# Kernel optimization log

Hardware: AMD Instinct MI355X
Metric: run time of the kernel (lower is better)

Reference implementation:

```python
import jax, jax.numpy as jnp
import numpy as np

N, IN, C, H, OUT = 100000, 64, 128, 2, 8
D = C // H  # per-head dim = 64
E = 600000
NEG_SLOPE = 0.2


def _edge_softmax(alpha, dst, n):
    # softmax over edges grouped by destination node; alpha: [E,H]
    amax = jax.lax.stop_gradient(jax.ops.segment_max(alpha, dst, num_segments=n))
    amax = jnp.where(jnp.isfinite(amax), amax, 0.0)  # empty segments -> -inf
    e = jnp.exp(alpha - amax[dst])
    s = jax.ops.segment_sum(e, dst, num_segments=n)
    return e / (s[dst] + 1e-16)


def _han_conv(x, edge_list, proj_w, proj_b, att_src, att_dst, q, kw, kb):
    # x: [N, F_in]; edge_list: list of [2,E] int arrays (one per edge type)
    n = x.shape[0]
    h = (x @ proj_w + proj_b).reshape(n, H, D)  # node-type projection
    outs = []
    for i, ei in enumerate(edge_list):  # loop over fixed set of edge types
        src, dst = ei[0], ei[1]
        a_src = (h * att_src[i]).sum(-1)  # [N,H]
        a_dst = (h * att_dst[i]).sum(-1)  # [N,H]
        alpha = jax.nn.leaky_relu(a_src[src] + a_dst[dst], NEG_SLOPE)  # [E,H]
        alpha = _edge_softmax(alpha, dst, n)  # dropout p=0.6 is identity in eval
        msg = h[src] * alpha[..., None]  # [E,H,D]
        out = jax.ops.segment_sum(msg, dst, num_segments=n).reshape(n, C)
        outs.append(jax.nn.relu(out))  # per-edge-type ReLU inside HANConv
    stacked = jnp.stack(outs)  # [M, N, C], M = num edge types
    # semantic-level attention across metapaths
    score = (q * jnp.tanh(stacked @ kw + kb).mean(1)).sum(-1)  # [M]
    attn = jax.nn.softmax(score)
    return (attn[:, None, None] * stacked).sum(0)  # [N, C]


def setup_inputs() -> dict:
    key = jax.random.key(0)
    ks = jax.random.split(key, 16)
    s = 0.1
    d = {}
    d["x"] = jax.random.normal(ks[0], (N, IN), jnp.float32)
    d["ei_spatial"] = jax.random.randint(ks[1], (2, E), 0, N)
    d["ei_similar"] = jax.random.randint(ks[2], (2, E), 0, N)
    # HANConv layer 1 (IN -> C)
    d["p1_proj_w"] = jax.random.normal(ks[3], (IN, C), jnp.float32) * s
    d["p1_proj_b"] = jnp.zeros((C,), jnp.float32)
    d["p1_att_src"] = jax.random.normal(ks[4], (2, H, D), jnp.float32) * s
    d["p1_att_dst"] = jax.random.normal(ks[5], (2, H, D), jnp.float32) * s
    d["p1_q"] = jax.random.normal(ks[6], (C,), jnp.float32) * s
    d["p1_kw"] = jax.random.normal(ks[7], (C, C), jnp.float32) * s
    d["p1_kb"] = jnp.zeros((C,), jnp.float32)
    # HANConv layer 2 (C -> C)
    d["p2_proj_w"] = jax.random.normal(ks[8], (C, C), jnp.float32) * s
    d["p2_proj_b"] = jnp.zeros((C,), jnp.float32)
    d["p2_att_src"] = jax.random.normal(ks[9], (2, H, D), jnp.float32) * s
    d["p2_att_dst"] = jax.random.normal(ks[10], (2, H, D), jnp.float32) * s
    d["p2_q"] = jax.random.normal(ks[11], (C,), jnp.float32) * s
    d["p2_kw"] = jax.random.normal(ks[12], (C, C), jnp.float32) * s
    d["p2_kb"] = jnp.zeros((C,), jnp.float32)
    # final classifier
    d["lin_w"] = jax.random.normal(ks[13], (C, OUT), jnp.float32) * s
    d["lin_b"] = jnp.zeros((OUT,), jnp.float32)
    return d


def reference(x, p1_proj_w, p1_proj_b, p1_att_src, p1_att_dst, p1_q, p1_kw, p1_kb,
              p2_proj_w, p2_proj_b, p2_att_src, p2_att_dst, p2_q, p2_kw, p2_kb,
              lin_w, lin_b, ei_spatial, ei_similar):
    edges = [ei_spatial, ei_similar]
    h = _han_conv(x, edges, p1_proj_w, p1_proj_b, p1_att_src, p1_att_dst, p1_q, p1_kw, p1_kb)
    h = jax.nn.relu(h)
    h = _han_conv(h, edges, p2_proj_w, p2_proj_b, p2_att_src, p2_att_dst, p2_q, p2_kw, p2_kb)
    h = jax.nn.relu(h)
    return h @ lin_w + lin_b  # [N, OUT]
```

## Files before the change

kernel.cpp:

```cpp
#include <hip/hip_runtime.h>

#define NNODES 100000
#define EEDGES 600000
#define CDIM 128
#define HHEADS 2
#define DDIM 64
#define FIN 64
#define FOUT 8
#define NEG 0.2f

#define SB 200
#define SCH 500
#define SNB 384
#define GEB 2344
#define CVB 448

typedef _Float16 f16x8 __attribute__((ext_vector_type(8)));
typedef unsigned short ushort8 __attribute__((ext_vector_type(8)));
typedef float f32x4 __attribute__((ext_vector_type(4)));

__device__ __forceinline__ float tanh_fast(float x) {
    float e = __expf(2.f * x);
    return 1.f - 2.f / (e + 1.f);
}

__device__ __forceinline__ unsigned short f2h(float x) {
    _Float16 h = (_Float16)x;
    return __builtin_bit_cast(unsigned short, h);
}
__device__ __forceinline__ float h2f(unsigned short u) {
    return (float)__builtin_bit_cast(_Float16, u);
}
__device__ __forceinline__ float hrelu2f(unsigned short u) {
    return (u & 0x8000) ? 0.f : (float)__builtin_bit_cast(_Float16, u);
}

__device__ __forceinline__ void attn_from_sacc(const float* saccp, float& fa0, float& fa1) {
    float s0 = saccp[0] / (float)NNODES;
    float s1 = saccp[1] / (float)NNODES;
    float m = fmaxf(s0, s1);
    float e0 = expf(s0 - m), e1 = expf(s1 - m);
    float inv = 1.f / (e0 + e1);
    fa0 = e0 * inv; fa1 = e1 * inv;
}

template<int K, int MODE>
__device__ __forceinline__
void proj_body(const void* __restrict__ Xv, const void* __restrict__ Xv2,
               const float* __restrict__ saccp,
               const unsigned short* __restrict__ pwT_b,
               const float* __restrict__ bias,
               const float* __restrict__ att_src, const float* __restrict__ att_dst,
               unsigned short* __restrict__ Hout,
               float* __restrict__ a_src, float* __restrict__ a_dst, int pbid) {
    const int U = K / 8;
    __shared__ ushort8 smem[192 * (K / 8)];
    ushort8* As8 = smem;
    ushort8* Bs8 = smem + 64 * U;
    int tid = threadIdx.x;
    int row0 = pbid * 64;
    float fa0 = 0.f, fa1 = 0.f;
    if (MODE == 2) attn_from_sacc(saccp, fa0, fa1);

#pragma unroll
    for (int i = 0; i < (64 * U) / 256; ++i) {
        int idx = tid + i * 256;
        int row = idx / U, u = idx % U;
        int grow = row0 + row;
        ushort8 v;
        if (grow < NNODES) {
            if (MODE == 2) {
                ushort8 v0 = ((const ushort8*)Xv)[(long)grow * U + u];
                ushort8 v1 = ((const ushort8*)Xv2)[(long)grow * U + u];
#pragma unroll
                for (int e = 0; e < 8; ++e)
                    v[e] = f2h(fa0 * hrelu2f(v0[e]) + fa1 * hrelu2f(v1[e]));
            } else {
                const float* p = (const float*)Xv + (long)grow * K + u * 8;
                float4 a = *(const float4*)p;
                float4 b = *(const float4*)(p + 4);
                v[0] = f2h(a.x); v[1] = f2h(a.y); v[2] = f2h(a.z); v[3] = f2h(a.w);
                v[4] = f2h(b.x); v[5] = f2h(b.y); v[6] = f2h(b.z); v[7] = f2h(b.w);
            }
        } else v = (ushort8)0;
        As8[row * U + (u ^ (row & 7))] = v;
    }
#pragma unroll
    for (int i = 0; i < (128 * U) / 256; ++i) {
        int idx = tid + i * 256;
        int c = idx / U, u = idx % U;
        Bs8[c * U + (u ^ (c & 7))] = ((const ushort8*)pwT_b)[idx];
    }
    __syncthreads();

    int l = tid & 63, w = tid >> 6;
    int lrow = w * 16 + (l & 15);
    int ug = l >> 4;
    f32x4 acc[8];
#pragma unroll
    for (int ct = 0; ct < 8; ++ct) acc[ct] = (f32x4)0.f;

#pragma unroll
    for (int kc = 0; kc < K / 32; ++kc) {
        int u = kc * 4 + ug;
        f16x8 af = __builtin_bit_cast(f16x8, As8[lrow * U + (u ^ (lrow & 7))]);
#pragma unroll
        for (int ct = 0; ct < 8; ++ct) {
            int c = ct * 16 + (l & 15);
            f16x8 bf = __builtin_bit_cast(f16x8, Bs8[c * U + (u ^ (c & 7))]);
            acc[ct] = __builtin_amdgcn_mfma_f32_16x16x32_f16(af, bf, acc[ct], 0, 0, 0);
        }
    }

    __syncthreads();
    unsigned short* Cs = (unsigned short*)smem;
#pragma unroll
    for (int ct = 0; ct < 8; ++ct) {
        int c = ct * 16 + (l & 15);
        float bc = bias[c];
#pragma unroll
        for (int v = 0; v < 4; ++v) {
            int rr = w * 16 + (l >> 4) * 4 + v;
            Cs[rr * 128 + c] = f2h(acc[ct][v] + bc);
        }
    }
    __syncthreads();

    int r = tid >> 2, q = tid & 3;
    int grow = row0 + r;
    if (grow < NNODES) {
        float h[32];
        ushort8 hv[4];
#pragma unroll
        for (int j = 0; j < 4; ++j) {
            hv[j] = *(ushort8*)&Cs[r * 128 + q * 32 + j * 8];
#pragma unroll
            for (int e = 0; e < 8; ++e) h[j * 8 + e] = h2f(hv[j][e]);
        }
#pragma unroll
        for (int j = 0; j < 4; ++j)
            *(ushort8*)(Hout + (long)grow * CDIM + q * 32 + j * 8) = hv[j];
#pragma unroll
        for (int i = 0; i < 2; ++i) {
            float s = 0.f, d = 0.f;
#pragma unroll
            for (int j = 0; j < 32; ++j) {
                s = fmaf(h[j], att_src[i * CDIM + q * 32 + j], s);
                d = fmaf(h[j], att_dst[i * CDIM + q * 32 + j], d);
            }
            s += __shfl_xor(s, 1, 64);
            d += __shfl_xor(d, 1, 64);
            if ((q & 1) == 0) {
                int hh = q >> 1;
                long base = (long)i * NNODES * HHEADS + (long)grow * HHEADS + hh;
                a_src[base] = s;
                a_dst[base] = d;
            }
        }
    }
}

__global__ __launch_bounds__(256)
void proj1_fill(const int* __restrict__ src0, const int* __restrict__ dst0,
                int* __restrict__ cur0, int* __restrict__ cs0,
                const int* __restrict__ src1, const int* __restrict__ dst1,
                int* __restrict__ cur1, int* __restrict__ cs1,
                const float* __restrict__ X,
                const unsigned short* __restrict__ pwT_b,
                const float* __restrict__ bias,
                const float* __restrict__ att_src, const float* __restrict__ att_dst,
                unsigned short* __restrict__ Hout,
                float* __restrict__ a_src, float* __restrict__ a_dst) {
    int bid = blockIdx.x;
    if (bid < 2 * GEB) {
        int type = bid >= GEB;
        const int* src = type ? src1 : src0;
        const int* dst = type ? dst1 : dst0;
        int* cursor = type ? cur1 : cur0;
        int* csr_src = type ? cs1 : cs0;
        int e = (bid - (type ? GEB : 0)) * 256 + threadIdx.x;
        if (e < EEDGES) {
            int pos = atomicAdd(&cursor[dst[e]], 1);
            csr_src[pos] = src[e];
        }
        return;
    }
    proj_body<FIN, 0>(X, nullptr, nullptr, pwT_b, bias, att_src, att_dst,
                      Hout, a_src, a_dst, bid - 2 * GEB);
}

__global__ __launch_bounds__(256)
void proj2_kernel(const void* __restrict__ Xv, const void* __restrict__ Xv2,
                  const float* __restrict__ saccp,
                  const unsigned short* __restrict__ pwT_b,
                  const float* __restrict__ bias,
                  const float* __restrict__ att_src, const float* __restrict__ att_dst,
                  unsigned short* __restrict__ Hout,
                  float* __restrict__ a_src, float* __restrict__ a_dst) {
    proj_body<CDIM, 2>(Xv, Xv2, saccp, pwT_b, bias, att_src, att_dst,
                       Hout, a_src, a_dst, blockIdx.x);
}

__global__ __launch_bounds__(256, 3)
void score_mfma_dual(const unsigned short* __restrict__ O0b,
                     const unsigned short* __restrict__ O1b,
                     const unsigned short* __restrict__ kwT_b,
                     const float* __restrict__ kb, const float* __restrict__ q,
                     float* __restrict__ sacc) {
    __shared__ ushort8 As8[64 * 16];
    __shared__ ushort8 Bs8[128 * 16];
    __shared__ float red[4];
    const int NT = (NNODES + 63) / 64;
    int bid = blockIdx.x;
    int type = bid >= SNB;
    const unsigned short* Omb = type ? O1b : O0b;
    int bt = bid - (type ? SNB : 0);
    int tid = threadIdx.x;

#pragma unroll
    for (int i = 0; i < 8; ++i) {
        int idx = tid + i * 256;
        int c = idx >> 4, u = idx & 15;
        Bs8[c * 16 + (u ^ (c & 7))] = ((const ushort8*)kwT_b)[idx];
    }

    int l = tid & 63, w = tid >> 6;
    int lrow = w * 16 + (l & 15);
    int ug = l >> 4;
    float s = 0.f;

    ushort8 pre[4];
    {
        int row0 = bt * 64;
#pragma unroll
        for (int i = 0; i < 4; ++i) {
            int idx = tid + i * 256;
            int row = idx >> 4, u = idx & 15;
            int grow = row0 + row;
            ushort8 v = (ushort8)0;
            if (bt < NT && grow < NNODES) {
                v = ((const ushort8*)Omb)[(long)grow * 16 + u];
#pragma unroll
                for (int e = 0; e < 8; ++e) v[e] = (v[e] & 0x8000) ? 0 : v[e];
            }
            pre[i] = v;
        }
    }

    for (int t = bt; t < NT; t += SNB) {
        __syncthreads();
#pragma unroll
        for (int i = 0; i < 4; ++i) {
            int idx = tid + i * 256;
            int row = idx >> 4, u = idx & 15;
            As8[row * 16 + (u ^ (row & 7))] = pre[i];
        }
        int tn = t + SNB;
        if (tn < NT) {
            int row0n = tn * 64;
#pragma unroll
            for (int i = 0; i < 4; ++i) {
                int idx = tid + i * 256;
                int row = idx >> 4, u = idx & 15;
                int grow = row0n + row;
                ushort8 v = (ushort8)0;
                if (grow < NNODES) {
                    v = ((const ushort8*)Omb)[(long)grow * 16 + u];
#pragma unroll
                    for (int e = 0; e < 8; ++e) v[e] = (v[e] & 0x8000) ? 0 : v[e];
                }
                pre[i] = v;
            }
        }
        __syncthreads();

        f32x4 acc[8];
#pragma unroll
        for (int ct = 0; ct < 8; ++ct) acc[ct] = (f32x4)0.f;
#pragma unroll
        for (int kc = 0; kc < 4; ++kc) {
            int u = kc * 4 + ug;
            f16x8 af = __builtin_bit_cast(f16x8, As8[lrow * 16 + (u ^ (lrow & 7))]);
#pragma unroll
            for (int ct = 0; ct < 8; ++ct) {
                int c = ct * 16 + (l & 15);
                f16x8 bf = __builtin_bit_cast(f16x8, Bs8[c * 16 + (u ^ (c & 7))]);
                acc[ct] = __builtin_amdgcn_mfma_f32_16x16x32_f16(af, bf, acc[ct], 0, 0, 0);
            }
        }
        int row0 = t * 64;
#pragma unroll
        for (int ct = 0; ct < 8; ++ct) {
            int c = ct * 16 + (l & 15);
            float qc = q[c], kbc = kb[c];
#pragma unroll
            for (int v = 0; v < 4; ++v) {
                int grow = row0 + w * 16 + (l >> 4) * 4 + v;
                if (grow < NNODES) s += qc * tanh_fast(acc[ct][v] + kbc);
            }
        }
    }

#pragma unroll
    for (int m = 32; m >= 1; m >>= 1) s += __shfl_xor(s, m, 64);
    if (l == 0) red[w] = s;
    __syncthreads();
    if (tid == 0) atomicAdd(sacc + type, red[0] + red[1] + red[2] + red[3]);
}

__global__ __launch_bounds__(256)
void hist_cvt(const int* __restrict__ dst0, int* __restrict__ deg0,
              const int* __restrict__ dst1, int* __restrict__ deg1,
              const float* __restrict__ p1w, const float* __restrict__ k1w,
              const float* __restrict__ p2w, const float* __restrict__ k2w,
              unsigned short* __restrict__ p1T, unsigned short* __restrict__ k1T,
              unsigned short* __restrict__ p2T, unsigned short* __restrict__ k2T,
              float* __restrict__ sacc) {
    int bid = blockIdx.x;
    if (bid < 2 * GEB) {
        int type = bid >= GEB;
        const int* dst = type ? dst1 : dst0;
        int* deg = type ? deg1 : deg0;
        int e = (bid - (type ? GEB : 0)) * 256 + threadIdx.x;
        if (e < EEDGES) atomicAdd(&deg[dst[e]], 1);
        return;
    }
    int idx = (bid - 2 * GEB) * 256 + threadIdx.x;
    if (bid == 2 * GEB && threadIdx.x < 4) sacc[threadIdx.x] = 0.f;
    if (idx < FIN * CDIM) {
        int c = idx / FIN, k = idx % FIN;
        p1T[idx] = f2h(p1w[k * CDIM + c]);
    } else if (idx < (FIN + CDIM) * CDIM) {
        int j = idx - FIN * CDIM;
        int c = j >> 7, k = j & 127;
        k1T[j] = f2h(k1w[k * CDIM + c]);
    } else if (idx < (FIN + 2 * CDIM) * CDIM) {
        int j = idx - (FIN + CDIM) * CDIM;
        int c = j >> 7, k = j & 127;
        p2T[j] = f2h(p2w[k * CDIM + c]);
    } else if (idx < (FIN + 3 * CDIM) * CDIM) {
        int j = idx - (FIN + 2 * CDIM) * CDIM;
        int c = j >> 7, k = j & 127;
        k2T[j] = f2h(k2w[k * CDIM + c]);
    }
}

__global__ __launch_bounds__(256)
void scan_partial_dual(const int* __restrict__ deg0, int* __restrict__ bsum0,
                       const int* __restrict__ deg1, int* __restrict__ bsum1) {
    __shared__ int red[256];
    int bid = blockIdx.x;
    int type = bid >= SB;
    const int* deg = type ? deg1 : deg0;
    int* bsum = type ? bsum1 : bsum0;
    int b = bid - (type ? SB : 0), t = threadIdx.x;
    int s = 0;
    if (t < 250) {
        int base = b * SCH + t * 2;
        s = deg[base] + deg[base + 1];
    }
    red[t] = s;
    __syncthreads();
#pragma unroll
    for (int off = 128; off >= 1; off >>= 1) {
        if (t < off) red[t] += red[t + off];
        __syncthreads();
    }
    if (t == 0) bsum[b] = red[0];
}

__global__ void scan_bsum_dual(int* __restrict__ bsum0, int* __restrict__ bsum1) {
    int t = threadIdx.x;
    if (t < 2) {
        int* bsum = t ? bsum1 : bsum0;
        int run = 0;
        for (int i = 0; i < SB; ++i) { int v = bsum[i]; bsum[i] = run; run += v; }
    }
}

__global__ __launch_bounds__(256)
void scan_final_dual(const int* __restrict__ deg0, const int* __restrict__ bsum0,
                     int* __restrict__ rowptr0, int* __restrict__ cursor0,
                     const int* __restrict__ deg1, const int* __restrict__ bsum1,
                     int* __restrict__ rowptr1, int* __restrict__ cursor1) {
    __shared__ int ts[256];
    int bid = blockIdx.x;
    int type = bid >= SB;
    const int* deg = type ? deg1 : deg0;
    const int* bsum = type ? bsum1 : bsum0;
    int* rowptr = type ? rowptr1 : rowptr0;
    int* cursor = type ? cursor1 : cursor0;
    int b = bid - (type ? SB : 0), t = threadIdx.x;
    int d0 = 0, d1 = 0;
    int base = b * SCH + t * 2;
    if (t < 250) { d0 = deg[base]; d1 = deg[base + 1]; }
    ts[t] = d0 + d1;
    __syncthreads();
#pragma unroll
    for (int off = 1; off < 256; off <<= 1) {
        int v = (t >= off) ? ts[t - off] : 0;
        __syncthreads();
        ts[t] += v;
        __syncthreads();
    }
    if (t < 250) {
        int excl = bsum[b] + (t > 0 ? ts[t - 1] : 0);
        rowptr[base] = excl;      cursor[base] = excl;
        rowptr[base + 1] = excl + d0;  cursor[base + 1] = excl + d0;
    }
    if (b == 0 && t == 0) rowptr[NNODES] = EEDGES;
}

__global__ __launch_bounds__(256)
void seg_aggregate_dual(const int* __restrict__ rp0, const int* __restrict__ cs0,
                        const float* __restrict__ as0, const float* __restrict__ ad0,
                        unsigned short* __restrict__ O0,
                        const int* __restrict__ rp1, const int* __restrict__ cs1,
                        const float* __restrict__ as1, const float* __restrict__ ad1,
                        unsigned short* __restrict__ O1,
                        const unsigned short* __restrict__ Hfeat, int gseg) {
    int bid = blockIdx.x;
    int type = bid >= gseg;
    const int* rowptr = type ? rp1 : rp0;
    const int* csr_src = type ? cs1 : cs0;
    const float* asv = type ? as1 : as0;
    const float* adv = type ? ad1 : ad0;
    unsigned short* Out = type ? O1 : O0;
    int wid = threadIdx.x >> 6;
    int lane = threadIdx.x & 63;
    int grp = lane >> 4;
    int cpos = lane & 15;
    int node = (bid - (type ? gseg : 0)) * 16 + wid * 4 + grp;
    int start = rowptr[node];
    int deg = rowptr[node + 1] - start;
    float2 adn = *(const float2*)(adv + node * 2);

    int md = max(deg, __shfl_xor(deg, 16, 64));
    md = max(md, __shfl_xor(md, 32, 64));

    float a[8] = {0.f, 0.f, 0.f, 0.f, 0.f, 0.f, 0.f, 0.f};
    float s0 = 0.f, s1 = 0.f;
    for (int i = 0; i < md; ++i) {
        if (i < deg) {
            int si = csr_src[start + i];
            float2 av = *(const float2*)(asv + si * 2);
            float r0 = av.x + adn.x; r0 = r0 >= 0.f ? r0 : NEG * r0;
            float r1 = av.y + adn.y; r1 = r1 >= 0.f ? r1 : NEG * r1;
            float w0 = __expf(r0), w1 = __expf(r1);
            s0 += w0; s1 += w1;
            float wsel = cpos < 8 ? w0 : w1;
            uint4 rh = *(const uint4*)(Hfeat + (long)si * CDIM + cpos * 8);
            f16x8 h = __builtin_bit_cast(f16x8, rh);
#pragma unroll
            for (int k = 0; k < 8; ++k) a[k] = fmaf((float)h[k], wsel, a[k]);
        }
    }
    float ssel = cpos < 8 ? s0 : s1;
    float inv = ssel > 0.f ? 1.f / ssel : 0.f;
    uint4 o;
    o.x = (unsigned int)f2h(a[0] * inv) | ((unsigned int)f2h(a[1] * inv) << 16);
    o.y = (unsigned int)f2h(a[2] * inv) | ((unsigned int)f2h(a[3] * inv) << 16);
    o.z = (unsigned int)f2h(a[4] * inv) | ((unsigned int)f2h(a[5] * inv) << 16);
    o.w = (unsigned int)f2h(a[6] * inv) | ((unsigned int)f2h(a[7] * inv) << 16);
    *(uint4*)(Out + (long)node * CDIM + cpos * 8) = o;
}

__global__ __launch_bounds__(256)
void final_linear_kernel(const unsigned short* __restrict__ O0,
                         const unsigned short* __restrict__ O1,
                         const float* __restrict__ saccp,
                         const float* __restrict__ lw, const float* __restrict__ lb,
                         float* __restrict__ out) {
    __shared__ float lws[CDIM * FOUT];
    int tid = threadIdx.x;
    for (int i = tid; i < CDIM * FOUT; i += 256) lws[i] = lw[i];
    __syncthreads();
    float fa0, fa1;
    attn_from_sacc(saccp, fa0, fa1);
    int idx = blockIdx.x * 256 + tid;
    if (idx >= NNODES * FOUT) return;
    int n = idx >> 3, o = idx & 7;
    const ushort8* r0 = (const ushort8*)(O0 + (long)n * CDIM);
    const ushort8* r1 = (const ushort8*)(O1 + (long)n * CDIM);
    float acc = lb[o];
#pragma unroll
    for (int k8 = 0; k8 < 16; ++k8) {
        ushort8 v0 = r0[k8];
        ushort8 v1 = r1[k8];
#pragma unroll
        for (int e = 0; e < 8; ++e) {
            float hv = fa0 * hrelu2f(v0[e]) + fa1 * hrelu2f(v1[e]);
            acc = fmaf(hv, lws[(k8 * 8 + e) * FOUT + o], acc);
        }
    }
    out[idx] = acc;
}

extern "C" void kernel_launch(void* const* d_in, const int* in_sizes, int n_in,
                              void* d_out, int out_size, void* d_ws, size_t ws_size,
                              hipStream_t stream) {
    const float* x          = (const float*)d_in[0];
    const int*   ei_spatial = (const int*)d_in[1];
    const int*   ei_similar = (const int*)d_in[2];
    const float* p1_proj_w  = (const float*)d_in[3];
    const float* p1_proj_b  = (const float*)d_in[4];
    const float* p1_att_src = (const float*)d_in[5];
    const float* p1_att_dst = (const float*)d_in[6];
    const float* p1_q       = (const float*)d_in[7];
    const float* p1_kw      = (const float*)d_in[8];
    const float* p1_kb      = (const float*)d_in[9];
    const float* p2_proj_w  = (const float*)d_in[10];
    const float* p2_proj_b  = (const float*)d_in[11];
    const float* p2_att_src = (const float*)d_in[12];
    const float* p2_att_dst = (const float*)d_in[13];
    const float* p2_q       = (const float*)d_in[14];
    const float* p2_kw      = (const float*)d_in[15];
    const float* p2_kb      = (const float*)d_in[16];
    const float* lin_w      = (const float*)d_in[17];
    const float* lin_b      = (const float*)d_in[18];

    float* ws = (float*)d_ws;
    const size_t nc = (size_t)NNODES * CDIM;
    const size_t nh2 = (size_t)NNODES * HHEADS;

    float* asrc = ws;
    float* adst = asrc + 2 * nh2;
    float* sacc = adst + 2 * nh2;
    int* rowptr0 = (int*)(sacc + 4);
    int* rowptr1 = rowptr0 + (NNODES + 1);
    int* cursor0 = rowptr1 + (NNODES + 1);
    int* cursor1 = cursor0 + (NNODES + 1);
    int* cs0     = cursor1 + (NNODES + 1);
    int* cs1     = cs0 + EEDGES;
    int* deg0    = cs1 + EEDGES;
    int* deg1    = deg0 + NNODES;
    int* bsum0   = deg1 + NNODES;
    int* bsum1   = bsum0 + SB;
    uintptr_t kp = (uintptr_t)(bsum1 + SB);
    kp = (kp + 15) & ~(uintptr_t)15;
    unsigned short* p1T = (unsigned short*)kp;
    unsigned short* k1T = p1T + FIN * CDIM;
    unsigned short* p2T = k1T + CDIM * CDIM;
    unsigned short* k2T = p2T + CDIM * CDIM;
    unsigned short* Hb  = k2T + CDIM * CDIM;
    unsigned short* O0b = Hb + nc;
    unsigned short* O1b = O0b + nc;

    const int gm = (NNODES + 63) / 64;
    const int gseg = NNODES / 16;
    const int nh = NNODES * HHEADS;

    hipMemsetAsync(deg0, 0, 2 * NNODES * sizeof(int), stream);
    hist_cvt<<<2 * GEB + CVB, 256, 0, stream>>>(
        ei_spatial + EEDGES, deg0, ei_similar + EEDGES, deg1,
        p1_proj_w, p1_kw, p2_proj_w, p2_kw, p1T, k1T, p2T, k2T, sacc);
    scan_partial_dual<<<2 * SB, 256, 0, stream>>>(deg0, bsum0, deg1, bsum1);
    scan_bsum_dual<<<1, 64, 0, stream>>>(bsum0, bsum1);
    scan_final_dual<<<2 * SB, 256, 0, stream>>>(deg0, bsum0, rowptr0, cursor0,
                                                deg1, bsum1, rowptr1, cursor1);

    proj1_fill<<<2 * GEB + gm, 256, 0, stream>>>(
        ei_spatial, ei_spatial + EEDGES, cursor0, cs0,
        ei_similar, ei_similar + EEDGES, cursor1, cs1,
        x, p1T, p1_proj_b, p1_att_src, p1_att_dst, Hb, asrc, adst);
    seg_aggregate_dual<<<2 * gseg, 256, 0, stream>>>(
        rowptr0, cs0, asrc, adst, O0b,
        rowptr1, cs1, asrc + nh, adst + nh, O1b, Hb, gseg);
    score_mfma_dual<<<2 * SNB, 256, 0, stream>>>(O0b, O1b, k1T, p1_kb, p1_q, sacc);

    proj2_kernel<<<gm, 256, 0, stream>>>(O0b, O1b, sacc, p2T, p2_proj_b,
                                         p2_att_src, p2_att_dst, Hb, asrc, adst);
    seg_aggregate_dual<<<2 * gseg, 256, 0, stream>>>(
        rowptr0, cs0, asrc, adst, O0b,
        rowptr1, cs1, asrc + nh, adst + nh, O1b, Hb, gseg);
    score_mfma_dual<<<2 * SNB, 256, 0, stream>>>(O0b, O1b, k2T, p2_kb, p2_q, sacc + 2);

    const int gfin = (NNODES * FOUT + 255) / 256;
    final_linear_kernel<<<gfin, 256, 0, stream>>>(O0b, O1b, sacc + 2, lin_w, lin_b,
                                                  (float*)d_out);
}
```

Measured before the change: 475.3 us.

## Build CSR via per-edge rank from histogram atomics instead of cursor atomics

The histogram kernel now records each edge's atomicAdd return value as its rank within its destination segment. A new atomic-free fill kernel scatters each source index to rowptr[dst]+rank, so the separate cursor array and the second pass of atomics are no longer needed. In exchange, the fill is split out of the fused proj1 launch into its own kernel, which adds a launch and writes and reads 4.8 MB of rank arrays.

Measured after the change: 411.0 us. 13.5% less time.

```diff
diff --git a/kernel.cpp b/kernel.cpp
--- a/kernel.cpp
+++ b/kernel.cpp
@@ -161,32 +161,14 @@
 }
 
 __global__ __launch_bounds__(256)
-void proj1_fill(const int* __restrict__ src0, const int* __restrict__ dst0,
-                int* __restrict__ cur0, int* __restrict__ cs0,
-                const int* __restrict__ src1, const int* __restrict__ dst1,
-                int* __restrict__ cur1, int* __restrict__ cs1,
-                const float* __restrict__ X,
-                const unsigned short* __restrict__ pwT_b,
-                const float* __restrict__ bias,
-                const float* __restrict__ att_src, const float* __restrict__ att_dst,
-                unsigned short* __restrict__ Hout,
-                float* __restrict__ a_src, float* __restrict__ a_dst) {
-    int bid = blockIdx.x;
-    if (bid < 2 * GEB) {
-        int type = bid >= GEB;
-        const int* src = type ? src1 : src0;
-        const int* dst = type ? dst1 : dst0;
-        int* cursor = type ? cur1 : cur0;
-        int* csr_src = type ? cs1 : cs0;
-        int e = (bid - (type ? GEB : 0)) * 256 + threadIdx.x;
-        if (e < EEDGES) {
-            int pos = atomicAdd(&cursor[dst[e]], 1);
-            csr_src[pos] = src[e];
-        }
-        return;
-    }
+void proj1_kernel(const float* __restrict__ X,
+                  const unsigned short* __restrict__ pwT_b,
+                  const float* __restrict__ bias,
+                  const float* __restrict__ att_src, const float* __restrict__ att_dst,
+                  unsigned short* __restrict__ Hout,
+                  float* __restrict__ a_src, float* __restrict__ a_dst) {
     proj_body<FIN, 0>(X, nullptr, nullptr, pwT_b, bias, att_src, att_dst,
-                      Hout, a_src, a_dst, bid - 2 * GEB);
+                      Hout, a_src, a_dst, blockIdx.x);
 }
 
 __global__ __launch_bounds__(256)
@@ -309,8 +291,8 @@
 }
 
 __global__ __launch_bounds__(256)
-void hist_cvt(const int* __restrict__ dst0, int* __restrict__ deg0,
-              const int* __restrict__ dst1, int* __restrict__ deg1,
+void hist_cvt(const int* __restrict__ dst0, int* __restrict__ deg0, int* __restrict__ rank0,
+              const int* __restrict__ dst1, int* __restrict__ deg1, int* __restrict__ rank1,
               const float* __restrict__ p1w, const float* __restrict__ k1w,
               const float* __restrict__ p2w, const float* __restrict__ k2w,
               unsigned short* __restrict__ p1T, unsigned short* __restrict__ k1T,
@@ -321,8 +303,9 @@
         int type = bid >= GEB;
         const int* dst = type ? dst1 : dst0;
         int* deg = type ? deg1 : deg0;
+        int* rank = type ? rank1 : rank0;
         int e = (bid - (type ? GEB : 0)) * 256 + threadIdx.x;
-        if (e < EEDGES) atomicAdd(&deg[dst[e]], 1);
+        if (e < EEDGES) rank[e] = atomicAdd(&deg[dst[e]], 1);
         return;
     }
     int idx = (bid - 2 * GEB) * 256 + threadIdx.x;
@@ -380,16 +363,15 @@
 
 __global__ __launch_bounds__(256)
 void scan_final_dual(const int* __restrict__ deg0, const int* __restrict__ bsum0,
-                     int* __restrict__ rowptr0, int* __restrict__ cursor0,
+                     int* __restrict__ rowptr0,
                      const int* __restrict__ deg1, const int* __restrict__ bsum1,
-                     int* __restrict__ rowptr1, int* __restrict__ cursor1) {
+                     int* __restrict__ rowptr1) {
     __shared__ int ts[256];
     int bid = blockIdx.x;
     int type = bid >= SB;
     const int* deg = type ? deg1 : deg0;
     const int* bsum = type ? bsum1 : bsum0;
     int* rowptr = type ? rowptr1 : rowptr0;
-    int* cursor = type ? cursor1 : cursor0;
     int b = bid - (type ? SB : 0), t = threadIdx.x;
     int d0 = 0, d1 = 0;
     int base = b * SCH + t * 2;
@@ -405,10 +387,31 @@
     }
     if (t < 250) {
         int excl = bsum[b] + (t > 0 ? ts[t - 1] : 0);
-        rowptr[base] = excl;      cursor[base] = excl;
-        rowptr[base + 1] = excl + d0;  cursor[base + 1] = excl + d0;
+        rowptr[base] = excl;
+        rowptr[base + 1] = excl + d0;
     }
     if (b == 0 && t == 0) rowptr[NNODES] = EEDGES;
+}
+
+__global__ __launch_bounds__(256)
+void fill_dual(const int* __restrict__ src0, const int* __restrict__ dst0,
+               const int* __restrict__ rank0, const int* __restrict__ rp0,
+               int* __restrict__ cs0,
+               const int* __restrict__ src1, const int* __restrict__ dst1,
+               const int* __restrict__ rank1, const int* __restrict__ rp1,
+               int* __restrict__ cs1) {
+    int bid = blockIdx.x;
+    int type = bid >= GEB;
+    const int* src = type ? src1 : src0;
+    const int* dst = type ? dst1 : dst0;
+    const int* rank = type ? rank1 : rank0;
+    const int* rowptr = type ? rp1 : rp0;
+    int* csr_src = type ? cs1 : cs0;
+    int e = (bid - (type ? GEB : 0)) * 256 + threadIdx.x;
+    if (e < EEDGES) {
+        int pos = rowptr[dst[e]] + rank[e];
+        csr_src[pos] = src[e];
+    }
 }
 
 __global__ __launch_bounds__(256)
@@ -528,9 +531,9 @@
     float* sacc = adst + 2 * nh2;
     int* rowptr0 = (int*)(sacc + 4);
     int* rowptr1 = rowptr0 + (NNODES + 1);
-    int* cursor0 = rowptr1 + (NNODES + 1);
-    int* cursor1 = cursor0 + (NNODES + 1);
-    int* cs0     = cursor1 + (NNODES + 1);
+    int* rank0   = rowptr1 + (NNODES + 1);
+    int* rank1   = rank0 + EEDGES;
+    int* cs0     = rank1 + EEDGES;
     int* cs1     = cs0 + EEDGES;
     int* deg0    = cs1 + EEDGES;
     int* deg1    = deg0 + NNODES;
@@ -552,17 +555,18 @@
 
     hipMemsetAsync(deg0, 0, 2 * NNODES * sizeof(int), stream);
     hist_cvt<<<2 * GEB + CVB, 256, 0, stream>>>(
-        ei_spatial + EEDGES, deg0, ei_similar + EEDGES, deg1,
+        ei_spatial + EEDGES, deg0, rank0, ei_similar + EEDGES, deg1, rank1,
         p1_proj_w, p1_kw, p2_proj_w, p2_kw, p1T, k1T, p2T, k2T, sacc);
     scan_partial_dual<<<2 * SB, 256, 0, stream>>>(deg0, bsum0, deg1, bsum1);
     scan_bsum_dual<<<1, 64, 0, stream>>>(bsum0, bsum1);
-    scan_final_dual<<<2 * SB, 256, 0, stream>>>(deg0, bsum0, rowptr0, cursor0,
-                                                deg1, bsum1, rowptr1, cursor1);
-
-    proj1_fill<<<2 * GEB + gm, 256, 0, stream>>>(
-        ei_spatial, ei_spatial + EEDGES, cursor0, cs0,
-        ei_similar, ei_similar + EEDGES, cursor1, cs1,
-        x, p1T, p1_proj_b, p1_att_src, p1_att_dst, Hb, asrc, adst);
+    scan_final_dual<<<2 * SB, 256, 0, stream>>>(deg0, bsum0, rowptr0,
+                                                deg1, bsum1, rowptr1);
+    fill_dual<<<2 * GEB, 256, 0, stream>>>(
+        ei_spatial, ei_spatial + EEDGES, rank0, rowptr0, cs0,
+        ei_similar, ei_similar + EEDGES, rank1, rowptr1, cs1);
+
+    proj1_kernel<<<gm, 256, 0, stream>>>(x, p1T, p1_proj_b, p1_att_src, p1_att_dst,
+                                         Hb, asrc, adst);
     seg_aggregate_dual<<<2 * gseg, 256, 0, stream>>>(
         rowptr0, cs0, asrc, adst, O0b,
         rowptr1, cs1, asrc + nh, adst + nh, O1b, Hb, gseg);
```
